# Optimization experiments

Hardware: AMD Instinct MI355X
Metric: run time of the kernel (lower is better)

## Reference

```python
import jax, jax.numpy as jnp
import numpy as np

B, N, C, H = 4, 1024, 768, 12
HD = C // H
EPS = 1e-5


def setup_inputs() -> dict:
    key = jax.random.key(0)
    ks = jax.random.split(key, 6)
    before = jax.random.normal(ks[0], (B, N, C), dtype=jnp.float32)
    after = jax.random.normal(ks[1], (B, N, C), dtype=jnp.float32)
    W_qkv = jax.random.normal(ks[2], (3 * C, C), dtype=jnp.float32) * (1.0 / np.sqrt(C))
    ln_g = jnp.ones((HD,), dtype=jnp.float32)
    ln_b = jnp.zeros((HD,), dtype=jnp.float32)
    W_proj = jax.random.normal(ks[3], (C, C), dtype=jnp.float32) * (1.0 / np.sqrt(C))
    b_proj = jnp.zeros((C,), dtype=jnp.float32)
    return {"before": before, "after": after, "W_qkv": W_qkv, "ln_g": ln_g,
            "ln_b": ln_b, "W_proj": W_proj, "b_proj": b_proj}


def _qkv_norm(x, W_qkv, ln_g, ln_b):
    # x: [B,N,C] -> qkv: [3,B,H,N,hd] with LayerNorm over head_dim
    qkv = (x @ W_qkv.T).reshape(B, N, 3, H, HD).transpose(2, 0, 3, 1, 4)
    mu = jnp.mean(qkv, axis=-1, keepdims=True)
    var = jnp.var(qkv, axis=-1, keepdims=True)
    qkv = (qkv - mu) * jax.lax.rsqrt(var + EPS) * ln_g + ln_b
    return qkv[0], qkv[1], qkv[2]


def _cross_attn(q, k, v, scale, W_proj, b_proj):
    # q,k,v: [B,H,N,hd]
    attn = jax.nn.softmax(jnp.einsum('bhqd,bhkd->bhqk', q, k) * scale, axis=-1)
    ctx = jnp.einsum('bhqk,bhkd->bhqd', attn, v)  # [B,H,N,hd]
    ctx = ctx.transpose(0, 2, 1, 3).reshape(B, N, C)
    ctx = ctx @ W_proj.T + b_proj
    # NOTE: original adds q.reshape(B,N,C) WITHOUT transposing heads back; replicate faithfully.
    return ctx + q.reshape(B, N, C)


def reference(before, after, W_qkv, ln_g, ln_b, W_proj, b_proj):
    scale = HD ** (-0.5)
    q_b, k_b, v_b = _qkv_norm(before, W_qkv, ln_g, ln_b)
    q_a, k_a, v_a = _qkv_norm(after, W_qkv, ln_g, ln_b)
    context_a = _cross_attn(q_b, k_a, v_a, scale, W_proj, b_proj)
    context_b = _cross_attn(q_a, k_b, v_b, scale, W_proj, b_proj)
    return (context_b, context_a)
```

## Files before the change

kernel.cpp:

```cpp
#include <hip/hip_runtime.h>


typedef __bf16 bf16x8 __attribute__((ext_vector_type(8)));
typedef float  f32x4  __attribute__((ext_vector_type(4)));
typedef unsigned int u32x4 __attribute__((ext_vector_type(4)));
typedef unsigned short us;

#define MFMA16(a, b, c) __builtin_amdgcn_mfma_f32_16x16x32_bf16(a, b, c, 0, 0, 0)

__device__ __forceinline__ us f2bf(float f) {
  unsigned int u = __builtin_bit_cast(unsigned int, f);
  u += 0x7FFFu + ((u >> 16) & 1u);
  return (us)(u >> 16);
}
__device__ __forceinline__ float bf2f(us h) {
  unsigned int u = ((unsigned int)h) << 16;
  return __builtin_bit_cast(float, u);
}
__device__ __forceinline__ bf16x8 ld16(const us* p) {
  return __builtin_bit_cast(bf16x8, *(const u32x4*)p);
}

#define CH 136

__global__ __launch_bounds__(256) void k_convert(
    const float* __restrict__ before, const float* __restrict__ after,
    const float* __restrict__ wqkv, const float* __restrict__ wproj,
    us* __restrict__ ws) {
  int t = blockIdx.x * 256 + threadIdx.x;
  us* dst; int u;
  if (t < 786432)       { u = t;           dst = ws; }
  else if (t < 1007616) { u = t - 786432;  dst = ws + 6291456; }
  else                  { u = t - 1007616; dst = ws + 8060928; }
  int l15 = u & 15, c2 = u >> 4;
  int kc = c2 % 96, mt = c2 / 96;
  int row = mt * 16 + l15;
  const float* srow;
  if (t < 786432)       srow = row < 4096 ? before + (size_t)row * 768
                                          : after + (size_t)(row - 4096) * 768;
  else if (t < 1007616) srow = wqkv + (size_t)row * 768;
  else                  srow = wproj + (size_t)row * 768;
  const float4* s4 = (const float4*)(srow + kc * 8);
  float4 a = s4[0], b = s4[1];
  union { u32x4 v; us s[8]; } o;
  o.s[0] = f2bf(a.x); o.s[1] = f2bf(a.y); o.s[2] = f2bf(a.z); o.s[3] = f2bf(a.w);
  o.s[4] = f2bf(b.x); o.s[5] = f2bf(b.y); o.s[6] = f2bf(b.z); o.s[7] = f2bf(b.w);
  *(u32x4*)(dst + (size_t)c2 * 128 + l15 * 8) = o.v;
}

template <int MT>
__device__ __forceinline__ void gemm_mainloop(
    const us* __restrict__ A, const us* __restrict__ B,
    int m0, int n0, us* As, us* Bs, f32x4 (&acc)[MT / 32][4]) {
  constexpr int AJ = MT / 32;
  constexpr int NITER = 12;
  const int tid = threadIdx.x, lane = tid & 63, w = tid >> 6;
  const int quad = lane >> 4, l15 = lane & 15;
  const int wm = (w >> 1) * (MT / 2), wn = (w & 1) * 64;
  u32x4 ra[AJ], rb[4];

  auto load_regs = [&](int k0) {
#pragma unroll
    for (int j = 0; j < AJ; ++j) {
      int u = w * AJ + j;
      ra[j] = *(const u32x4*)(A + ((size_t)((m0 >> 4) + (u >> 1)) * 96
                                   + (k0 >> 3) + (u & 1) * 4) * 128 + lane * 8);
    }
#pragma unroll
    for (int j = 0; j < 4; ++j) {
      int u = w * 4 + j;
      rb[j] = *(const u32x4*)(B + ((size_t)((n0 >> 4) + (u >> 1)) * 96
                                   + (k0 >> 3) + (u & 1) * 4) * 128 + lane * 8);
    }
  };
  auto store_regs = [&]() {
#pragma unroll
    for (int j = 0; j < AJ; ++j) {
      int slot = (w * AJ + j) * 4 + quad;
      *(u32x4*)(As + slot * CH + l15 * 8) = ra[j];
    }
#pragma unroll
    for (int j = 0; j < 4; ++j) {
      int slot = (w * 4 + j) * 4 + quad;
      *(u32x4*)(Bs + slot * CH + l15 * 8) = rb[j];
    }
  };

  load_regs(0);
  store_regs();
  __syncthreads();

#pragma unroll
  for (int it = 0; it < NITER; ++it) {
    if (it + 1 < NITER) load_regs((it + 1) * 64);
#pragma unroll
    for (int ks = 0; ks < 2; ++ks) {
      bf16x8 af[AJ], bfr[4];
#pragma unroll
      for (int mf = 0; mf < AJ; ++mf)
        af[mf] = ld16(As + (((wm >> 4) + mf) * 8 + ks * 4 + quad) * CH + l15 * 8);
#pragma unroll
      for (int nf = 0; nf < 4; ++nf)
        bfr[nf] = ld16(Bs + (((wn >> 4) + nf) * 8 + ks * 4 + quad) * CH + l15 * 8);
#pragma unroll
      for (int mf = 0; mf < AJ; ++mf)
#pragma unroll
        for (int nf = 0; nf < 4; ++nf)
          acc[mf][nf] = MFMA16(af[mf], bfr[nf], acc[mf][nf]);
    }
    __syncthreads();
    if (it + 1 < NITER) {
      store_regs();
      __syncthreads();
    }
  }
}

__global__ __launch_bounds__(256) void k_gemm_qkv(
    const us* __restrict__ A, const us* __restrict__ B, us* __restrict__ Cqk,
    us* __restrict__ Vg, const float* __restrict__ g, const float* __restrict__ bb) {
  __shared__ us As[64 * CH];
  __shared__ us Bs[64 * CH];
  const int lane = threadIdx.x & 63, w = threadIdx.x >> 6;
  const int quad = lane >> 4, l15 = lane & 15;
  const int m0 = blockIdx.x * 128, n0 = blockIdx.y * 128;
  const int wm = (w >> 1) * 64, wn = (w & 1) * 64;
  f32x4 acc[4][4] = {};
  gemm_mainloop<128>(A, B, m0, n0, As, Bs, acc);

  float gl[4], bl[4];
#pragma unroll
  for (int nf = 0; nf < 4; ++nf) { gl[nf] = g[nf * 16 + l15]; bl[nf] = bb[nf * 16 + l15]; }

  if ((n0 + wn) < 1536) {
#pragma unroll
    for (int mf = 0; mf < 4; ++mf)
#pragma unroll
      for (int r = 0; r < 4; ++r) {
        float s1 = acc[mf][0][r] + acc[mf][1][r] + acc[mf][2][r] + acc[mf][3][r];
        float s2 = acc[mf][0][r] * acc[mf][0][r] + acc[mf][1][r] * acc[mf][1][r]
                 + acc[mf][2][r] * acc[mf][2][r] + acc[mf][3][r] * acc[mf][3][r];
#pragma unroll
        for (int o = 1; o < 16; o <<= 1) { s1 += __shfl_xor(s1, o); s2 += __shfl_xor(s2, o); }
        float mu = s1 * (1.0f / 64.0f);
        float var = s2 * (1.0f / 64.0f) - mu * mu;
        float sc = rsqrtf(var + 1e-5f);
        size_t cb = ((size_t)(((m0 + wm) >> 4) + mf) * 192 + ((n0 + wn) >> 3)
                     + (l15 >> 3)) * 128 + (quad * 4 + r) * 8 + (l15 & 7);
#pragma unroll
        for (int nf = 0; nf < 4; ++nf)
          Cqk[cb + nf * 256] = f2bf((acc[mf][nf][r] - mu) * sc * gl[nf] + bl[nf]);
      }
  } else {
    const int h = ((n0 + wn) - 1536) >> 6;
#pragma unroll
    for (int mf = 0; mf < 4; ++mf) {
      int mrow = m0 + wm + mf * 16;
      int s = mrow >> 12, b2 = (mrow >> 10) & 3;
      int K0 = mrow & 1023;
      us* vb = Vg + (size_t)(s * 48 + b2 * 12 + h) * 65536;
      float vv[4][4];
#pragma unroll
      for (int r = 0; r < 4; ++r) {
        float s1 = acc[mf][0][r] + acc[mf][1][r] + acc[mf][2][r] + acc[mf][3][r];
        float s2 = acc[mf][0][r] * acc[mf][0][r] + acc[mf][1][r] * acc[mf][1][r]
                 + acc[mf][2][r] * acc[mf][2][r] + acc[mf][3][r] * acc[mf][3][r];
#pragma unroll
        for (int o = 1; o < 16; o <<= 1) { s1 += __shfl_xor(s1, o); s2 += __shfl_xor(s2, o); }
        float mu = s1 * (1.0f / 64.0f);
        float var = s2 * (1.0f / 64.0f) - mu * mu;
        float sc = rsqrtf(var + 1e-5f);
#pragma unroll
        for (int nf = 0; nf < 4; ++nf)
          vv[nf][r] = (acc[mf][nf][r] - mu) * sc * gl[nf] + bl[nf];
      }
#pragma unroll
      for (int nf = 0; nf < 4; ++nf) {
        ushort4 o4;
        o4.x = f2bf(vv[nf][0]); o4.y = f2bf(vv[nf][1]);
        o4.z = f2bf(vv[nf][2]); o4.w = f2bf(vv[nf][3]);
        *(ushort4*)(vb + ((size_t)nf * 128 + (K0 >> 3) + (quad >> 1)) * 128
                    + l15 * 8 + (quad & 1) * 4) = o4;
      }
    }
  }
}

__global__ __launch_bounds__(256) void k_gemm_proj(
    const us* __restrict__ A, const us* __restrict__ B, float* __restrict__ C,
    const us* __restrict__ qkvr, const float* __restrict__ bias) {
  __shared__ us As[32 * CH];
  __shared__ us Bs[64 * CH];
  const int lane = threadIdx.x & 63, w = threadIdx.x >> 6;
  const int quad = lane >> 4, l15 = lane & 15;
  const int m0 = blockIdx.x * 64, n0 = blockIdx.y * 128;
  const int wm = (w >> 1) * 32, wn = (w & 1) * 64;
  f32x4 acc[2][4] = {};
  gemm_mainloop<64>(A, B, m0, n0, As, Bs, acc);

  const int cg = (n0 + wn) >> 6;
  float bl[4];
#pragma unroll
  for (int nf = 0; nf < 4; ++nf) bl[nf] = bias[n0 + wn + nf * 16 + l15];
#pragma unroll
  for (int mf = 0; mf < 2; ++mf)
#pragma unroll
    for (int r = 0; r < 4; ++r) {
      int row = m0 + wm + mf * 16 + quad * 4 + r;
      int hf = row >> 12;
      int m4 = row & 4095;
      int b = m4 >> 10, i = m4 & 1023;
      int j = i * 12 + cg;
      int h = j >> 10, n = j & 1023;
      int qrow = ((hf ^ 1) << 12) + (b << 10) + n;
      size_t rb2 = ((size_t)(qrow >> 4) * 192 + h * 8 + (l15 >> 3)) * 128
                 + (qrow & 15) * 8 + (l15 & 7);
      size_t base = (size_t)row * 768 + n0 + wn + l15;
#pragma unroll
      for (int nf = 0; nf < 4; ++nf)
        C[base + nf * 16] = acc[mf][nf][r] + bl[nf] + bf2f(qkvr[rb2 + nf * 256]);
    }
}

__global__ __launch_bounds__(256) void k_attn(const us* __restrict__ qkvr,
                                              const us* __restrict__ vtg,
                                              us* __restrict__ ctx) {
  __shared__ us Ks[2][32 * CH];
  __shared__ us Vt[2][32 * CH];
  __shared__ us Ps[4][32 * 72];
  const int tid = threadIdx.x, lane = tid & 63, w = tid >> 6;
  const int quad = lane >> 4, l15 = lane & 15;
  const int hi = blockIdx.x, qt = blockIdx.y;
  const int hf = hi / 48, bh = hi - hf * 48;
  const int b = bh / 12, h = bh - (bh / 12) * 12;
  const int ihq = hf ^ 1, ihk = hf;
  const int r0 = qt * 128 + w * 32;
  const int qmt = (ihq * 4096 + b * 1024 + r0) >> 4;
  const int kb16 = (ihk * 4096 + b * 1024) >> 4;
  const us* vbase = vtg + (size_t)(ihk * 48 + b * 12 + h) * 65536;
  const float c1 = 0.125f * 1.44269504088896340736f;

  bf16x8 aq[2][2];
#pragma unroll
  for (int mf = 0; mf < 2; ++mf)
#pragma unroll
    for (int ks = 0; ks < 2; ++ks)
      aq[mf][ks] = ld16(qkvr + ((size_t)(qmt + mf) * 192 + h * 8 + ks * 4 + quad) * 128
                        + l15 * 8);

  u32x4 rk[2], rv[2];
  auto load_kv = [&](int kt) {
#pragma unroll
    for (int j = 0; j < 2; ++j) {
      int u = w * 2 + j;
      rk[j] = *(const u32x4*)(qkvr + ((size_t)(kb16 + kt * 4 + (u >> 1)) * 192
                                      + 96 + h * 8 + (u & 1) * 4) * 128 + lane * 8);
      rv[j] = *(const u32x4*)(vbase + ((size_t)(u >> 1) * 128 + kt * 8
                                       + (u & 1) * 4) * 128 + lane * 8);
    }
  };
  auto store_kv = [&](int buf) {
#pragma unroll
    for (int j = 0; j < 2; ++j) {
      int slot = (w * 2 + j) * 4 + quad;
      *(u32x4*)(Ks[buf] + slot * CH + l15 * 8) = rk[j];
      *(u32x4*)(Vt[buf] + slot * CH + l15 * 8) = rv[j];
    }
  };

  f32x4 O[2][4] = {};
  float lsum[2][4] = {};
  us* myP = Ps[w];

  load_kv(0);
  store_kv(0);
  __syncthreads();

  for (int kt = 0; kt < 16; ++kt) {
    const int p = kt & 1;
    if (kt + 1 < 16) load_kv(kt + 1);

    f32x4 s[2][4] = {};
#pragma unroll
    for (int ks = 0; ks < 2; ++ks)
#pragma unroll
      for (int nf = 0; nf < 4; ++nf) {
        bf16x8 bk = ld16(Ks[p] + (nf * 8 + ks * 4 + quad) * CH + l15 * 8);
        s[0][nf] = MFMA16(aq[0][ks], bk, s[0][nf]);
        s[1][nf] = MFMA16(aq[1][ks], bk, s[1][nf]);
      }

#pragma unroll
    for (int mf = 0; mf < 2; ++mf)
#pragma unroll
      for (int r = 0; r < 4; ++r) {
        float p0 = __builtin_amdgcn_exp2f(s[mf][0][r] * c1);
        float p1 = __builtin_amdgcn_exp2f(s[mf][1][r] * c1);
        float p2 = __builtin_amdgcn_exp2f(s[mf][2][r] * c1);
        float p3 = __builtin_amdgcn_exp2f(s[mf][3][r] * c1);
        lsum[mf][r] += (p0 + p1) + (p2 + p3);
        int rowq = (mf * 16 + quad * 4 + r) * 72 + l15;
        myP[rowq]      = f2bf(p0);
        myP[rowq + 16] = f2bf(p1);
        myP[rowq + 32] = f2bf(p2);
        myP[rowq + 48] = f2bf(p3);
      }

#pragma unroll
    for (int k2 = 0; k2 < 2; ++k2) {
      bf16x8 pa0 = ld16(myP + l15 * 72 + k2 * 32 + quad * 8);
      bf16x8 pa1 = ld16(myP + (16 + l15) * 72 + k2 * 32 + quad * 8);
#pragma unroll
      for (int df = 0; df < 4; ++df) {
        bf16x8 bv = ld16(Vt[p] + (df * 8 + k2 * 4 + quad) * CH + l15 * 8);
        O[0][df] = MFMA16(pa0, bv, O[0][df]);
        O[1][df] = MFMA16(pa1, bv, O[1][df]);
      }
    }

    if (kt + 1 < 16) store_kv(p ^ 1);
    __syncthreads();
  }

  const int omt = (hf * 4096 + b * 1024 + r0) >> 4;
#pragma unroll
  for (int mf = 0; mf < 2; ++mf)
#pragma unroll
    for (int r = 0; r < 4; ++r) {
      float l = lsum[mf][r];
#pragma unroll
      for (int o = 1; o < 16; o <<= 1) l += __shfl_xor(l, o);
      float inv = 1.0f / l;
      size_t cb = ((size_t)(omt + mf) * 96 + h * 8 + (l15 >> 3)) * 128
                + (quad * 4 + r) * 8 + (l15 & 7);
#pragma unroll
      for (int df = 0; df < 4; ++df)
        ctx[cb + df * 256] = f2bf(O[mf][df][r] * inv);
    }
}

extern "C" void kernel_launch(void* const* d_in, const int* in_sizes, int n_in,
                              void* d_out, int out_size, void* d_ws, size_t ws_size,
                              hipStream_t stream) {
  (void)in_sizes; (void)n_in; (void)out_size; (void)ws_size;
  const float* before = (const float*)d_in[0];
  const float* after  = (const float*)d_in[1];
  const float* wqkv   = (const float*)d_in[2];
  const float* lng    = (const float*)d_in[3];
  const float* lnb    = (const float*)d_in[4];
  const float* wproj  = (const float*)d_in[5];
  const float* bproj  = (const float*)d_in[6];
  float* out = (float*)d_out;
  us* ws  = (us*)d_ws;
  us* xbt  = ws;
  us* wqt  = ws + 6291456;
  us* wpt  = ws + 8060928;
  us* qkvr = ws + 8650752;
  us* vtg  = ws + 21233664;
  us* ctx  = ws + 27525120;

  k_convert<<<4224, 256, 0, stream>>>(before, after, wqkv, wproj, ws);
  k_gemm_qkv<<<dim3(64, 18), 256, 0, stream>>>(xbt, wqt, qkvr, vtg, lng, lnb);
  k_attn<<<dim3(96, 8), 256, 0, stream>>>(qkvr, vtg, ctx);
  k_gemm_proj<<<dim3(128, 6), 256, 0, stream>>>(ctx, wpt, out, qkvr, bproj);
}
```

Baseline: 198.7 us.

## Keep softmax probabilities in registers via transposed MFMA and fold scale into Q

The attention kernel now computes S transposed (K as the A operand), so the exp2 outputs land in registers in the layout the PV MFMA needs as its B operand. This removes the per-tile LDS round trip for P and the Ps shared buffer. The V tile layout written by the QKV GEMM is permuted to match the new operand order. The softmax scale times log2(e) is folded into Q in the QKV epilogue, and the projection epilogue undoes it when adding the q residual. The price is an extra bf16 rounding on the scaled Q and the residual path.

```diff
diff --git a/kernel.cpp b/kernel.cpp
--- a/kernel.cpp
+++ b/kernel.cpp
@@ -8,6 +8,9 @@
 
 #define MFMA16(a, b, c) __builtin_amdgcn_mfma_f32_16x16x32_bf16(a, b, c, 0, 0, 0)
 
+#define C1F 0.18033688011112042f
+#define INV_C1F 5.545177444479562f
+
 __device__ __forceinline__ us f2bf(float f) {
   unsigned int u = __builtin_bit_cast(unsigned int, f);
   u += 0x7FFFu + ((u >> 16) & 1u);
@@ -19,6 +22,11 @@
 }
 __device__ __forceinline__ bf16x8 ld16(const us* p) {
   return __builtin_bit_cast(bf16x8, *(const u32x4*)p);
+}
+__device__ __forceinline__ unsigned int pkbf(float lo, float hi) {
+  return __builtin_amdgcn_perm(__builtin_bit_cast(unsigned int, hi),
+                               __builtin_bit_cast(unsigned int, lo),
+                               0x07060302u);
 }
 
 #define CH 136
@@ -133,6 +141,7 @@
   for (int nf = 0; nf < 4; ++nf) { gl[nf] = g[nf * 16 + l15]; bl[nf] = bb[nf * 16 + l15]; }
 
   if ((n0 + wn) < 1536) {
+    const float qs = (n0 + wn) < 768 ? C1F : 1.0f;
 #pragma unroll
     for (int mf = 0; mf < 4; ++mf)
 #pragma unroll
@@ -149,7 +158,7 @@
                      + (l15 >> 3)) * 128 + (quad * 4 + r) * 8 + (l15 & 7);
 #pragma unroll
         for (int nf = 0; nf < 4; ++nf)
-          Cqk[cb + nf * 256] = f2bf((acc[mf][nf][r] - mu) * sc * gl[nf] + bl[nf]);
+          Cqk[cb + nf * 256] = f2bf(((acc[mf][nf][r] - mu) * sc * gl[nf] + bl[nf]) * qs);
       }
   } else {
     const int h = ((n0 + wn) - 1536) >> 6;
@@ -158,6 +167,7 @@
       int mrow = m0 + wm + mf * 16;
       int s = mrow >> 12, b2 = (mrow >> 10) & 3;
       int K0 = mrow & 1023;
+      int nfk = (K0 >> 4) & 3;
       us* vb = Vg + (size_t)(s * 48 + b2 * 12 + h) * 65536;
       float vv[4][4];
 #pragma unroll
@@ -174,13 +184,14 @@
         for (int nf = 0; nf < 4; ++nf)
           vv[nf][r] = (acc[mf][nf][r] - mu) * sc * gl[nf] + bl[nf];
       }
+      size_t pchunk = ((size_t)(K0 >> 6) << 3) + ((nfk >> 1) << 2) + quad;
+      int poff = l15 * 8 + (nfk & 1) * 4;
 #pragma unroll
       for (int nf = 0; nf < 4; ++nf) {
         ushort4 o4;
         o4.x = f2bf(vv[nf][0]); o4.y = f2bf(vv[nf][1]);
         o4.z = f2bf(vv[nf][2]); o4.w = f2bf(vv[nf][3]);
-        *(ushort4*)(vb + ((size_t)nf * 128 + (K0 >> 3) + (quad >> 1)) * 128
-                    + l15 * 8 + (quad & 1) * 4) = o4;
+        *(ushort4*)(vb + ((size_t)nf * 128 + pchunk) * 128 + poff) = o4;
       }
     }
   }
@@ -218,7 +229,7 @@
       size_t base = (size_t)row * 768 + n0 + wn + l15;
 #pragma unroll
       for (int nf = 0; nf < 4; ++nf)
-        C[base + nf * 16] = acc[mf][nf][r] + bl[nf] + bf2f(qkvr[rb2 + nf * 256]);
+        C[base + nf * 16] = acc[mf][nf][r] + bl[nf] + bf2f(qkvr[rb2 + nf * 256]) * INV_C1F;
     }
 }
 
@@ -227,7 +238,6 @@
                                               us* __restrict__ ctx) {
   __shared__ us Ks[2][32 * CH];
   __shared__ us Vt[2][32 * CH];
-  __shared__ us Ps[4][32 * 72];
   const int tid = threadIdx.x, lane = tid & 63, w = tid >> 6;
   const int quad = lane >> 4, l15 = lane & 15;
   const int hi = blockIdx.x, qt = blockIdx.y;
@@ -238,7 +248,6 @@
   const int qmt = (ihq * 4096 + b * 1024 + r0) >> 4;
   const int kb16 = (ihk * 4096 + b * 1024) >> 4;
   const us* vbase = vtg + (size_t)(ihk * 48 + b * 12 + h) * 65536;
-  const float c1 = 0.125f * 1.44269504088896340736f;
 
   bf16x8 aq[2][2];
 #pragma unroll
@@ -269,8 +278,7 @@
   };
 
   f32x4 O[2][4] = {};
-  float lsum[2][4] = {};
-  us* myP = Ps[w];
+  float lsum[2] = {};
 
   load_kv(0);
   store_kv(0);
@@ -280,63 +288,69 @@
     const int p = kt & 1;
     if (kt + 1 < 16) load_kv(kt + 1);
 
-    f32x4 s[2][4] = {};
+    f32x4 sT[2][4] = {};
 #pragma unroll
     for (int ks = 0; ks < 2; ++ks)
 #pragma unroll
       for (int nf = 0; nf < 4; ++nf) {
-        bf16x8 bk = ld16(Ks[p] + (nf * 8 + ks * 4 + quad) * CH + l15 * 8);
-        s[0][nf] = MFMA16(aq[0][ks], bk, s[0][nf]);
-        s[1][nf] = MFMA16(aq[1][ks], bk, s[1][nf]);
-      }
-
-#pragma unroll
-    for (int mf = 0; mf < 2; ++mf)
-#pragma unroll
-      for (int r = 0; r < 4; ++r) {
-        float p0 = __builtin_amdgcn_exp2f(s[mf][0][r] * c1);
-        float p1 = __builtin_amdgcn_exp2f(s[mf][1][r] * c1);
-        float p2 = __builtin_amdgcn_exp2f(s[mf][2][r] * c1);
-        float p3 = __builtin_amdgcn_exp2f(s[mf][3][r] * c1);
-        lsum[mf][r] += (p0 + p1) + (p2 + p3);
-        int rowq = (mf * 16 + quad * 4 + r) * 72 + l15;
-        myP[rowq]      = f2bf(p0);
-        myP[rowq + 16] = f2bf(p1);
-        myP[rowq + 32] = f2bf(p2);
-        myP[rowq + 48] = f2bf(p3);
-      }
-
-#pragma unroll
-    for (int k2 = 0; k2 < 2; ++k2) {
-      bf16x8 pa0 = ld16(myP + l15 * 72 + k2 * 32 + quad * 8);
-      bf16x8 pa1 = ld16(myP + (16 + l15) * 72 + k2 * 32 + quad * 8);
+        bf16x8 kf = ld16(Ks[p] + (nf * 8 + ks * 4 + quad) * CH + l15 * 8);
+        sT[0][nf] = MFMA16(kf, aq[0][ks], sT[0][nf]);
+        sT[1][nf] = MFMA16(kf, aq[1][ks], sT[1][nf]);
+      }
+
+    bf16x8 pf[2][2];
+#pragma unroll
+    for (int mf = 0; mf < 2; ++mf) {
+      float ev[4][4];
+#pragma unroll
+      for (int nf = 0; nf < 4; ++nf)
+#pragma unroll
+        for (int r = 0; r < 4; ++r)
+          ev[nf][r] = __builtin_amdgcn_exp2f(sT[mf][nf][r]);
+      lsum[mf] += ((ev[0][0] + ev[0][1]) + (ev[0][2] + ev[0][3]))
+                + ((ev[1][0] + ev[1][1]) + (ev[1][2] + ev[1][3]))
+                + ((ev[2][0] + ev[2][1]) + (ev[2][2] + ev[2][3]))
+                + ((ev[3][0] + ev[3][1]) + (ev[3][2] + ev[3][3]));
+#pragma unroll
+      for (int k2 = 0; k2 < 2; ++k2) {
+        u32x4 wds;
+#pragma unroll
+        for (int wd = 0; wd < 4; ++wd)
+          wds[wd] = pkbf(ev[k2 * 2 + (wd >> 1)][(wd & 1) * 2],
+                         ev[k2 * 2 + (wd >> 1)][(wd & 1) * 2 + 1]);
+        pf[mf][k2] = __builtin_bit_cast(bf16x8, wds);
+      }
+    }
+
+#pragma unroll
+    for (int k2 = 0; k2 < 2; ++k2)
 #pragma unroll
       for (int df = 0; df < 4; ++df) {
-        bf16x8 bv = ld16(Vt[p] + (df * 8 + k2 * 4 + quad) * CH + l15 * 8);
-        O[0][df] = MFMA16(pa0, bv, O[0][df]);
-        O[1][df] = MFMA16(pa1, bv, O[1][df]);
-      }
-    }
+        bf16x8 av = ld16(Vt[p] + (df * 8 + k2 * 4 + quad) * CH + l15 * 8);
+        O[0][df] = MFMA16(av, pf[0][k2], O[0][df]);
+        O[1][df] = MFMA16(av, pf[1][k2], O[1][df]);
+      }
 
     if (kt + 1 < 16) store_kv(p ^ 1);
     __syncthreads();
   }
 
-  const int omt = (hf * 4096 + b * 1024 + r0) >> 4;
-#pragma unroll
-  for (int mf = 0; mf < 2; ++mf)
-#pragma unroll
-    for (int r = 0; r < 4; ++r) {
-      float l = lsum[mf][r];
-#pragma unroll
-      for (int o = 1; o < 16; o <<= 1) l += __shfl_xor(l, o);
-      float inv = 1.0f / l;
-      size_t cb = ((size_t)(omt + mf) * 96 + h * 8 + (l15 >> 3)) * 128
-                + (quad * 4 + r) * 8 + (l15 & 7);
-#pragma unroll
-      for (int df = 0; df < 4; ++df)
-        ctx[cb + df * 256] = f2bf(O[mf][df][r] * inv);
-    }
+  const int mc0 = hf * 256 + b * 64 + qt * 8 + w * 2;
+#pragma unroll
+  for (int mf = 0; mf < 2; ++mf) {
+    float l = lsum[mf];
+    l += __shfl_xor(l, 16);
+    l += __shfl_xor(l, 32);
+    float inv = 1.0f / l;
+#pragma unroll
+    for (int df = 0; df < 4; ++df) {
+      ushort4 o4;
+      o4.x = f2bf(O[mf][df][0] * inv); o4.y = f2bf(O[mf][df][1] * inv);
+      o4.z = f2bf(O[mf][df][2] * inv); o4.w = f2bf(O[mf][df][3] * inv);
+      *(ushort4*)(ctx + ((size_t)(mc0 + mf) * 96 + h * 8 + df * 2 + (quad >> 1)) * 128
+                  + l15 * 8 + (quad & 1) * 4) = o4;
+    }
+  }
 }
 
 extern "C" void kernel_launch(void* const* d_in, const int* in_sizes, int n_in,
```

Result: faster. 189.6 us (-4.6%).
